# Kernel tuning notes

Measured on AMD Instinct MI355X. Metric: run time of the kernel, lower is better.

Reference implementation:

```python
import jax, jax.numpy as jnp
import numpy as np
import math

DIM = 1024
H = 16
DH = DIM // H
B = 2
L = 1024


def setup_inputs() -> dict:
    key = jax.random.key(0)
    ks = jax.random.split(key, 8)
    s = 1.0 / math.sqrt(DIM)
    return {
        "Q": jax.random.normal(ks[0], (B, L, DIM), jnp.float32),
        "K": jax.random.normal(ks[1], (B, L, DIM), jnp.float32),
        "mask_Q": jax.random.bernoulli(ks[2], 0.1, (B, L)),
        "mask_K": jax.random.bernoulli(ks[3], 0.1, (B, L)),
        "Wq": jax.random.normal(ks[4], (DIM, DIM), jnp.float32) * s,
        "Wk": jax.random.normal(ks[5], (DIM, DIM), jnp.float32) * s,
        "Wv": jax.random.normal(ks[6], (DIM, DIM), jnp.float32) * s,
        "Wo": jax.random.normal(ks[7], (DIM, DIM), jnp.float32) * s,
    }


def reference(Q, K, mask_Q, mask_K, Wq, Wk, Wv, Wo):
    # V defaults to K. Masked positions of inputs are zeroed first.
    Qz = jnp.where(mask_Q[:, :, None], 0.0, Q)
    Kz = jnp.where(mask_K[:, :, None], 0.0, K)
    Vz = Kz  # V = K, masked with mask_K

    # Projections (nn.Linear, no bias): y = x @ W.T
    Qp = jnp.einsum('bld,ed->ble', Qz, Wq)
    Kp = jnp.einsum('bld,ed->ble', Kz, Wk)
    Vp = jnp.einsum('bld,ed->ble', Vz, Wv)

    # split heads: [B, L, H, DH] -> per-head attention
    qh = Qp.reshape(B, L, H, DH)
    kh = Kp.reshape(B, L, H, DH)
    vh = Vp.reshape(B, L, H, DH)

    # NOTE: original scales by sqrt(dim) (full dim), not sqrt(dim_split)
    scores = jnp.einsum('bqhd,bkhd->bhqk', qh, kh) / math.sqrt(DIM)

    # outer-product validity mask: valid iff both q and k positions unmasked
    valid = (~mask_Q)[:, None, :, None] & (~mask_K)[:, None, None, :]  # [B,1,Lq,Lk]
    A = jnp.where(valid, scores, -1e38)
    A = jax.nn.softmax(A, axis=-1)
    A = jnp.where(valid, A, 0.0)

    O = jnp.einsum('bhqk,bkhd->bqhd', A, vh).reshape(B, L, DIM)
    # residual uses the PROJECTED Q (Q was reassigned to fc_q(Q) in torch)
    O = Qp + O
    # masked_forward(fc_o, ...): fc_o applied, masked query rows forced to 0
    ff = jax.nn.relu(jnp.where(mask_Q[:, :, None], 0.0, jnp.einsum('bld,ed->ble', O, Wo)))
    O = O + ff
    return O
```

## Files before the change

kernel.cpp:

```cpp
#include <hip/hip_runtime.h>
#include <hip/hip_bf16.h>


#define DEV __device__ __forceinline__

typedef __attribute__((ext_vector_type(8))) short bf16x8;
typedef __attribute__((ext_vector_type(4))) float f32x4;
typedef __hip_bfloat16 bf16;

DEV void glds16(const bf16* g, bf16* s) {
  __builtin_amdgcn_global_load_lds(
      (const __attribute__((address_space(1))) void*)g,
      (__attribute__((address_space(3))) void*)s, 16, 0, 0);
}

DEV unsigned short f2bu(float x) {
  __hip_bfloat16 b = __float2bfloat16(x);
  unsigned short u;
  __builtin_memcpy(&u, &b, 2);
  return u;
}

DEV float bu2f(unsigned short u) {
  unsigned int v = (unsigned int)u << 16;
  float f;
  __builtin_memcpy(&f, &v, 4);
  return f;
}

__global__ __launch_bounds__(256) void cast_all(
    const float* __restrict__ Q, const float* __restrict__ K,
    const unsigned char* __restrict__ mq_raw, const unsigned char* __restrict__ mk_raw,
    const float* __restrict__ W0, const float* __restrict__ W1,
    const float* __restrict__ W2, const float* __restrict__ W3,
    bf16* __restrict__ Qz, bf16* __restrict__ Kz,
    bf16* __restrict__ o0, bf16* __restrict__ o1,
    bf16* __restrict__ o2, bf16* __restrict__ o3,
    unsigned char* __restrict__ mqn,
    unsigned long long* __restrict__ qm64, unsigned long long* __restrict__ km64) {
  __shared__ int cnt;
  const int z = blockIdx.z;
  const int t = threadIdx.x;
  if (z < 2) {
    const float* X = z ? K : Q;
    const unsigned char* raw = z ? mk_raw : mq_raw;
    bf16* out = z ? Kz : Qz;
    if (t == 0) cnt = 0;
    __syncthreads();
    int c = 0;
#pragma unroll
    for (int j = 0; j < 8; ++j) c += (raw[t * 8 + j] != 0);
    atomicAdd(&cnt, c);
    __syncthreads();
    const bool isByte = cnt > 128;
    int i = (blockIdx.x * 256 + t) * 8;
    int row = i >> 10;
    bool masked = isByte ? (raw[row] != 0) : (((const int*)raw)[row] != 0);
    float4 v0 = *(const float4*)&X[i];
    float4 v1 = *(const float4*)&X[i + 4];
    if (masked) {
      v0 = make_float4(0.f, 0.f, 0.f, 0.f);
      v1 = make_float4(0.f, 0.f, 0.f, 0.f);
    }
    *(ushort4*)&out[i] = make_ushort4(f2bu(v0.x), f2bu(v0.y), f2bu(v0.z), f2bu(v0.w));
    *(ushort4*)&out[i + 4] = make_ushort4(f2bu(v1.x), f2bu(v1.y), f2bu(v1.z), f2bu(v1.w));
  } else if (z < 6) {
    if (blockIdx.x >= 512) return;
    const float* X; bf16* out;
    switch (z) {
      case 2: X = W0; out = o0; break;
      case 3: X = W1; out = o1; break;
      case 4: X = W2; out = o2; break;
      default: X = W3; out = o3; break;
    }
    int i = (blockIdx.x * 256 + t) * 8;
    float4 v0 = *(const float4*)&X[i];
    float4 v1 = *(const float4*)&X[i + 4];
    *(ushort4*)&out[i] = make_ushort4(f2bu(v0.x), f2bu(v0.y), f2bu(v0.z), f2bu(v0.w));
    *(ushort4*)&out[i + 4] = make_ushort4(f2bu(v1.x), f2bu(v1.y), f2bu(v1.z), f2bu(v1.w));
  } else {
    if (blockIdx.x != 0) return;
    if (t == 0) cnt = 0;
    __syncthreads();
    int c = 0;
    for (int i = t; i < 2048; i += 256) c += (mq_raw[i] != 0);
    atomicAdd(&cnt, c);
    __syncthreads();
    const bool isByte = cnt > 128;
    for (int i = t; i < 2048; i += 256)
      mqn[i] = isByte ? (mq_raw[i] != 0) : (((const int*)mq_raw)[i] != 0);
    if (t < 64) {
      const unsigned char* src = (t < 32) ? mk_raw : mq_raw;
      int idx = t & 31;
      unsigned long long m = 0;
      for (int j = 0; j < 64; ++j) {
        int pos = idx * 64 + j;
        bool bit = isByte ? (src[pos] != 0) : (((const int*)src)[pos] != 0);
        m |= (unsigned long long)bit << j;
      }
      if (t < 32) km64[idx] = m; else qm64[idx] = m;
    }
  }
}

template <int MI, int NI, typename EPI>
DEV void gemm_core(const bf16* __restrict__ A, const bf16* __restrict__ W,
                   int K, int brow, int bcol, EPI&& epi) {
  __shared__ bf16 As[2 * MI * 512];
  __shared__ bf16 Bs[2 * NI * 2048];
  const int t = threadIdx.x, l = t & 63, w = t >> 6;
  const int rs = l >> 2;
  const int kcol = (l & 3) * 8;

  f32x4 acc[MI][NI];
#pragma unroll
  for (int i = 0; i < MI; i++)
#pragma unroll
    for (int j = 0; j < NI; j++) acc[i][j] = (f32x4){0.f, 0.f, 0.f, 0.f};

  auto stage = [&](int k0, int b_) {
#pragma unroll
    for (int i = 0; i < MI; ++i)
      if ((i & 3) == w)
        glds16(A + (size_t)(brow + i * 16 + rs) * K + k0 + kcol,
               &As[b_ * MI * 512 + i * 512]);
#pragma unroll
    for (int c = 0; c < NI; ++c)
      glds16(W + (size_t)(bcol + (w * NI + c) * 16 + rs) * K + k0 + kcol,
             &Bs[b_ * NI * 2048 + (w * NI + c) * 512]);
  };

  const int aoff0 = (l & 15) * 32 + (l >> 4) * 8;
  const int boff0 = (w * NI * 16 + (l & 15)) * 32 + (l >> 4) * 8;

  stage(0, 0);
  int buf = 0;
  for (int k0 = 0; k0 < K; k0 += 32) {
    __syncthreads();
    if (k0 + 32 < K) stage(k0 + 32, buf ^ 1);
    bf16x8 a[MI], b[NI];
#pragma unroll
    for (int mi = 0; mi < MI; ++mi)
      a[mi] = *(const bf16x8*)&As[buf * MI * 512 + aoff0 + mi * 512];
#pragma unroll
    for (int ni = 0; ni < NI; ++ni)
      b[ni] = *(const bf16x8*)&Bs[buf * NI * 2048 + boff0 + ni * 512];
#pragma unroll
    for (int mi = 0; mi < MI; ++mi)
#pragma unroll
      for (int ni = 0; ni < NI; ++ni)
        acc[mi][ni] = __builtin_amdgcn_mfma_f32_16x16x32_bf16(a[mi], b[ni], acc[mi][ni], 0, 0, 0);
    buf ^= 1;
  }

#pragma unroll
  for (int mi = 0; mi < MI; ++mi)
#pragma unroll
    for (int ni = 0; ni < NI; ++ni)
#pragma unroll
      for (int r = 0; r < 4; ++r) {
        int row = brow + mi * 16 + (l >> 4) * 4 + r;
        int col = bcol + (w * NI + ni) * 16 + (l & 15);
        epi(row, col, acc[mi][ni][r]);
      }
}

__global__ __launch_bounds__(256) void proj_gemm(
    const bf16* __restrict__ Qz, const bf16* __restrict__ Kz,
    const bf16* __restrict__ Wq, const bf16* __restrict__ Wk, const bf16* __restrict__ Wv,
    bf16* __restrict__ Qpb, bf16* __restrict__ Kpb, bf16* __restrict__ Vpb) {
  const int z = blockIdx.z;
  const int brow = blockIdx.x * 32, bcol = blockIdx.y * 128;
  const bf16* A = (z == 0) ? Qz : Kz;
  const bf16* W = (z == 0) ? Wq : ((z == 1) ? Wk : Wv);
  bf16* dst = (z == 0) ? Qpb : ((z == 1) ? Kpb : Vpb);
  const float scale = (z == 0) ? 0.045084220f : 1.0f;
  gemm_core<2, 2>(A, W, 1024, brow, bcol, [&](int row, int col, float v) {
    dst[((size_t)row << 10) + col] = __float2bfloat16(v * scale);
  });
}

__global__ __launch_bounds__(256) void final_gemm(
    const bf16* __restrict__ Ob, const bf16* __restrict__ Wo,
    float* __restrict__ out, const unsigned char* __restrict__ mq) {
  const int brow = blockIdx.x * 32, bcol = blockIdx.y * 64;
  gemm_core<2, 1>(Ob, Wo, 1024, brow, bcol, [&](int row, int col, float v) {
    size_t idx = ((size_t)row << 10) + col;
    float ff = mq[row] ? 0.f : fmaxf(v, 0.f);
    out[idx] = out[idx] + ff;
  });
}

__global__ __launch_bounds__(512) void attn_fused(
    const bf16* __restrict__ Qpb, const bf16* __restrict__ Kpb, const bf16* __restrict__ Vpb,
    const unsigned long long* __restrict__ qm64, const unsigned long long* __restrict__ km64,
    float* __restrict__ Of, bf16* __restrict__ Ob) {
  __shared__ bf16 Klds[2][2][64 * 64];
  __shared__ bf16 Vt[2][64 * 72];
  __shared__ float CombO[256][17];
  __shared__ float CombP[256];

  const int t = threadIdx.x, l = t & 63, w = t >> 6;
  const int kg = w >> 2, wq = w & 3;
  const int tg = t & 255;
  const int q = l & 15, g = l >> 4;
  const int f = blockIdx.x;
  const int bh = (f & 7) + 8 * ((f >> 3) & 3);
  const int qt = f >> 5;
  const int b = bh >> 4, h = bh & 15;
  const size_t bbase = (size_t)b * 1024;

  const int qg = qt * 64 + wq * 16 + q;
  const bf16* qptr = Qpb + (bbase + qg) * 1024 + h * 64 + g * 8;
  const bf16x8 qb0 = *(const bf16x8*)qptr;
  const bf16x8 qb1 = *(const bf16x8*)(qptr + 32);

  float psum = 0.f;
  f32x4 oacc[4];
#pragma unroll
  for (int mf = 0; mf < 4; ++mf) oacc[mf] = (f32x4){0.f, 0.f, 0.f, 0.f};

  const int krow_s = l >> 3;
  const int kcol_s = ((l & 7) ^ krow_s) * 8;
  const int vk0 = 2 * (tg & 31);
  const int vdc = tg >> 5;

  union { uint4 v; unsigned short s[8]; } u0, u1;

  auto stageK = [&](int kt_, int b_) {
#pragma unroll
    for (int c = 0; c < 2; ++c) {
      int cw = wq * 2 + c;
      glds16(Kpb + (bbase + kt_ * 64 + cw * 8 + krow_s) * 1024 + h * 64 + kcol_s,
             &Klds[kg][b_][cw * 512]);
    }
  };
  auto loadV = [&](int kt_) {
    const bf16* g0 = Vpb + (bbase + kt_ * 64 + vk0) * 1024 + h * 64 + vdc * 8;
    u0.v = *(const uint4*)g0;
    u1.v = *(const uint4*)(g0 + 1024);
  };

  stageK(kg * 8, 0);
  loadV(kg * 8);
  int buf = 0;

  for (int it = 0; it < 8; ++it) {
    const int kt = kg * 8 + it;
    const unsigned long long km = km64[b * 16 + kt];
    const unsigned long long mloc = km >> (4 * g);

    __syncthreads();

#pragma unroll
    for (int j = 0; j < 8; ++j) {
      unsigned int pk = (unsigned int)u0.s[j] | ((unsigned int)u1.s[j] << 16);
      *(unsigned int*)((char*)&Vt[kg][0] + (vdc * 8 + j) * 144 + vk0 * 2) = pk;
    }

    f32x4 S[4];
#pragma unroll
    for (int mf = 0; mf < 4; ++mf) {
#pragma unroll
      for (int r = 0; r < 4; ++r)
        S[mf][r] = ((mloc >> (mf * 16 + r)) & 1ull) ? -1e30f : 0.f;
      const int row = mf * 16 + q;
      const int rowb = row * 128;
      const bf16x8 ka0 = *(const bf16x8*)((const char*)&Klds[kg][buf][0] + rowb + ((g ^ (row & 7)) * 16));
      const bf16x8 ka1 = *(const bf16x8*)((const char*)&Klds[kg][buf][0] + rowb + (((g + 4) ^ (row & 7)) * 16));
      S[mf] = __builtin_amdgcn_mfma_f32_16x16x32_bf16(ka0, qb0, S[mf], 0, 0, 0);
      S[mf] = __builtin_amdgcn_mfma_f32_16x16x32_bf16(ka1, qb1, S[mf], 0, 0, 0);
    }

    unsigned int lo[4], hi[4];
#pragma unroll
    for (int mf = 0; mf < 4; ++mf) {
      float p0 = exp2f(S[mf][0]), p1 = exp2f(S[mf][1]);
      float p2 = exp2f(S[mf][2]), p3 = exp2f(S[mf][3]);
      psum += (p0 + p1) + (p2 + p3);
      lo[mf] = (unsigned int)f2bu(p0) | ((unsigned int)f2bu(p1) << 16);
      hi[mf] = (unsigned int)f2bu(p2) | ((unsigned int)f2bu(p3) << 16);
    }

    __syncthreads();

    if (it < 7) {
      stageK(kt + 1, buf ^ 1);
      loadV(kt + 1);
    }

    const int srcA = ((2 * g) & 3) * 16 + q;
    const int srcB = srcA + 16;
    const bool sel = (g >> 1) & 1;
#pragma unroll
    for (int ks = 0; ks < 2; ++ks) {
      unsigned int a0 = __shfl(lo[2 * ks], srcA), a1 = __shfl(hi[2 * ks], srcA);
      unsigned int a2 = __shfl(lo[2 * ks], srcB), a3 = __shfl(hi[2 * ks], srcB);
      unsigned int b0 = __shfl(lo[2 * ks + 1], srcA), b1 = __shfl(hi[2 * ks + 1], srcA);
      unsigned int b2 = __shfl(lo[2 * ks + 1], srcB), b3 = __shfl(hi[2 * ks + 1], srcB);
      uint4 pw;
      pw.x = sel ? b0 : a0; pw.y = sel ? b1 : a1;
      pw.z = sel ? b2 : a2; pw.w = sel ? b3 : a3;
      const bf16x8 pa = __builtin_bit_cast(bf16x8, pw);
#pragma unroll
      for (int mf = 0; mf < 4; ++mf) {
        const bf16x8 va = *(const bf16x8*)((const char*)&Vt[kg][0] + (mf * 16 + q) * 144 + ks * 64 + g * 16);
        oacc[mf] = __builtin_amdgcn_mfma_f32_16x16x32_bf16(va, pa, oacc[mf], 0, 0, 0);
      }
    }
    buf ^= 1;
  }

  __syncthreads();
  if (t >= 256) {
#pragma unroll
    for (int mf = 0; mf < 4; ++mf)
#pragma unroll
      for (int r = 0; r < 4; ++r) CombO[tg][mf * 4 + r] = oacc[mf][r];
    CombP[tg] = psum;
  }
  __syncthreads();
  if (t < 256) {
#pragma unroll
    for (int mf = 0; mf < 4; ++mf)
#pragma unroll
      for (int r = 0; r < 4; ++r) oacc[mf][r] += CombO[t][mf * 4 + r];
    psum += CombP[t];
    psum += __shfl_xor(psum, 16);
    psum += __shfl_xor(psum, 32);

    const unsigned long long qm = qm64[b * 16 + qt];
    const bool qvalid = !((qm >> (wq * 16 + q)) & 1ull);
    const float inv = (qvalid && psum > 0.f) ? 1.f / psum : 0.f;
    const float RQ = 22.180709777918f;
#pragma unroll
    for (int mf = 0; mf < 4; ++mf) {
      size_t idx = (bbase + qg) * 1024 + h * 64 + mf * 16 + g * 4;
      ushort4 q4 = *(const ushort4*)&Qpb[idx];
      float4 val;
      val.x = bu2f(q4.x) * RQ + oacc[mf][0] * inv;
      val.y = bu2f(q4.y) * RQ + oacc[mf][1] * inv;
      val.z = bu2f(q4.z) * RQ + oacc[mf][2] * inv;
      val.w = bu2f(q4.w) * RQ + oacc[mf][3] * inv;
      *(float4*)&Of[idx] = val;
      *(ushort4*)&Ob[idx] = make_ushort4(f2bu(val.x), f2bu(val.y), f2bu(val.z), f2bu(val.w));
    }
  }
}

extern "C" void kernel_launch(void* const* d_in, const int* in_sizes, int n_in,
                              void* d_out, int out_size, void* d_ws, size_t ws_size,
                              hipStream_t stream) {
  const float* Q = (const float*)d_in[0];
  const float* K = (const float*)d_in[1];
  const unsigned char* mQraw = (const unsigned char*)d_in[2];
  const unsigned char* mKraw = (const unsigned char*)d_in[3];
  const float* Wq = (const float*)d_in[4];
  const float* Wk = (const float*)d_in[5];
  const float* Wv = (const float*)d_in[6];
  const float* Wo = (const float*)d_in[7];
  float* out = (float*)d_out;

  char* ws = (char*)d_ws;
  const size_t MB = 1024 * 1024;
  bf16* Qz = (bf16*)(ws + 0);
  bf16* Kz = (bf16*)(ws + 4 * MB);
  bf16* Wqb = (bf16*)(ws + 8 * MB);
  bf16* Wkb = (bf16*)(ws + 10 * MB);
  bf16* Wvb = (bf16*)(ws + 12 * MB);
  bf16* Wob = (bf16*)(ws + 14 * MB);
  bf16* Qpb = (bf16*)(ws + 16 * MB);
  bf16* Kpb = (bf16*)(ws + 20 * MB);
  bf16* Vpb = (bf16*)(ws + 24 * MB);
  bf16* Ob  = (bf16*)(ws + 28 * MB);
  unsigned char* mqn = (unsigned char*)(ws + 32 * MB);
  unsigned long long* km64 = (unsigned long long*)(ws + 32 * MB + 4096);
  unsigned long long* qm64 = km64 + 32;

  dim3 gc(1024, 1, 7);
  cast_all<<<gc, 256, 0, stream>>>(Q, K, mQraw, mKraw, Wq, Wk, Wv, Wo,
                                   Qz, Kz, Wqb, Wkb, Wvb, Wob, mqn, qm64, km64);

  dim3 gp(64, 8, 3);
  proj_gemm<<<gp, 256, 0, stream>>>(Qz, Kz, Wqb, Wkb, Wvb, Qpb, Kpb, Vpb);

  attn_fused<<<512, 512, 0, stream>>>(Qpb, Kpb, Vpb, qm64, km64, out, Ob);

  dim3 gf(64, 16);
  final_gemm<<<gf, 256, 0, stream>>>(Ob, Wob, out, mqn);
}
```

Before: 104.5 us.

## Retile projection and output GEMMs, add XCD-aware block mapping, drop attention key split

The projection GEMM moves to 128x128 tiles with 4x4 MFMA per wave, and the output GEMM to 64x64 tiles. Both use a 1D grid remapped so neighbouring tiles land on the same XCD. The attention kernel drops the two-way key split and its LDS combine step, running 256 threads over all 16 key tiles, and s_setprio is placed around the MFMA blocks. The aim is more operand reuse per tile, better L2 locality and no reduction overhead. The cost is fewer blocks in flight and longer serial loops in attention.

```diff
diff --git a/kernel.cpp b/kernel.cpp
--- a/kernel.cpp
+++ b/kernel.cpp
@@ -103,106 +103,141 @@
   }
 }
 
-template <int MI, int NI, typename EPI>
-DEV void gemm_core(const bf16* __restrict__ A, const bf16* __restrict__ W,
-                   int K, int brow, int bcol, EPI&& epi) {
-  __shared__ bf16 As[2 * MI * 512];
-  __shared__ bf16 Bs[2 * NI * 2048];
-  const int t = threadIdx.x, l = t & 63, w = t >> 6;
-  const int rs = l >> 2;
-  const int kcol = (l & 3) * 8;
-
-  f32x4 acc[MI][NI];
-#pragma unroll
-  for (int i = 0; i < MI; i++)
-#pragma unroll
-    for (int j = 0; j < NI; j++) acc[i][j] = (f32x4){0.f, 0.f, 0.f, 0.f};
-
-  auto stage = [&](int k0, int b_) {
-#pragma unroll
-    for (int i = 0; i < MI; ++i)
-      if ((i & 3) == w)
-        glds16(A + (size_t)(brow + i * 16 + rs) * K + k0 + kcol,
-               &As[b_ * MI * 512 + i * 512]);
-#pragma unroll
-    for (int c = 0; c < NI; ++c)
-      glds16(W + (size_t)(bcol + (w * NI + c) * 16 + rs) * K + k0 + kcol,
-             &Bs[b_ * NI * 2048 + (w * NI + c) * 512]);
-  };
-
-  const int aoff0 = (l & 15) * 32 + (l >> 4) * 8;
-  const int boff0 = (w * NI * 16 + (l & 15)) * 32 + (l >> 4) * 8;
-
-  stage(0, 0);
-  int buf = 0;
-  for (int k0 = 0; k0 < K; k0 += 32) {
-    __syncthreads();
-    if (k0 + 32 < K) stage(k0 + 32, buf ^ 1);
-    bf16x8 a[MI], b[NI];
-#pragma unroll
-    for (int mi = 0; mi < MI; ++mi)
-      a[mi] = *(const bf16x8*)&As[buf * MI * 512 + aoff0 + mi * 512];
-#pragma unroll
-    for (int ni = 0; ni < NI; ++ni)
-      b[ni] = *(const bf16x8*)&Bs[buf * NI * 2048 + boff0 + ni * 512];
-#pragma unroll
-    for (int mi = 0; mi < MI; ++mi)
-#pragma unroll
-      for (int ni = 0; ni < NI; ++ni)
-        acc[mi][ni] = __builtin_amdgcn_mfma_f32_16x16x32_bf16(a[mi], b[ni], acc[mi][ni], 0, 0, 0);
-    buf ^= 1;
-  }
-
-#pragma unroll
-  for (int mi = 0; mi < MI; ++mi)
-#pragma unroll
-    for (int ni = 0; ni < NI; ++ni)
-#pragma unroll
-      for (int r = 0; r < 4; ++r) {
-        int row = brow + mi * 16 + (l >> 4) * 4 + r;
-        int col = bcol + (w * NI + ni) * 16 + (l & 15);
-        epi(row, col, acc[mi][ni][r]);
-      }
-}
-
 __global__ __launch_bounds__(256) void proj_gemm(
     const bf16* __restrict__ Qz, const bf16* __restrict__ Kz,
     const bf16* __restrict__ Wq, const bf16* __restrict__ Wk, const bf16* __restrict__ Wv,
     bf16* __restrict__ Qpb, bf16* __restrict__ Kpb, bf16* __restrict__ Vpb) {
-  const int z = blockIdx.z;
-  const int brow = blockIdx.x * 32, bcol = blockIdx.y * 128;
+  __shared__ bf16 As[2][128 * 32];
+  __shared__ bf16 Bs[2][128 * 32];
+  const int raw = blockIdx.x;
+  const int xcd = raw & 7, idx = raw >> 3;
+  const int x = idx & 15;
+  const int g = (idx >> 4) * 8 + xcd;
+  const int y = g & 7, z = g >> 3;
   const bf16* A = (z == 0) ? Qz : Kz;
   const bf16* W = (z == 0) ? Wq : ((z == 1) ? Wk : Wv);
   bf16* dst = (z == 0) ? Qpb : ((z == 1) ? Kpb : Vpb);
   const float scale = (z == 0) ? 0.045084220f : 1.0f;
-  gemm_core<2, 2>(A, W, 1024, brow, bcol, [&](int row, int col, float v) {
-    dst[((size_t)row << 10) + col] = __float2bfloat16(v * scale);
-  });
+  const int brow = x * 128, bcol = y * 128;
+
+  const int t = threadIdx.x, l = t & 63, w = t >> 6;
+  const int wr = w >> 1, wc = w & 1;
+  const int rA0 = w * 32 + (l >> 2);
+  const int kcol = (l & 3) * 8;
+
+  f32x4 acc[4][4];
+#pragma unroll
+  for (int i = 0; i < 4; i++)
+#pragma unroll
+    for (int j = 0; j < 4; j++) acc[i][j] = (f32x4){0.f, 0.f, 0.f, 0.f};
+
+  auto stage = [&](int k0, int b_) {
+#pragma unroll
+    for (int c = 0; c < 2; ++c) {
+      glds16(A + (size_t)(brow + rA0 + c * 16) * 1024 + k0 + kcol,
+             &As[b_][w * 1024 + c * 512]);
+      glds16(W + (size_t)(bcol + rA0 + c * 16) * 1024 + k0 + kcol,
+             &Bs[b_][w * 1024 + c * 512]);
+    }
+  };
+
+  const int aoff = (wr * 64 + (l & 15)) * 32 + (l >> 4) * 8;
+  const int boff = (wc * 64 + (l & 15)) * 32 + (l >> 4) * 8;
+
+  stage(0, 0);
+  int buf = 0;
+  for (int k0 = 0; k0 < 1024; k0 += 32) {
+    __syncthreads();
+    if (k0 + 32 < 1024) stage(k0 + 32, buf ^ 1);
+    bf16x8 a[4], b[4];
+#pragma unroll
+    for (int mi = 0; mi < 4; ++mi) a[mi] = *(const bf16x8*)&As[buf][aoff + mi * 512];
+#pragma unroll
+    for (int ni = 0; ni < 4; ++ni) b[ni] = *(const bf16x8*)&Bs[buf][boff + ni * 512];
+    __builtin_amdgcn_s_setprio(1);
+#pragma unroll
+    for (int mi = 0; mi < 4; ++mi)
+#pragma unroll
+      for (int ni = 0; ni < 4; ++ni)
+        acc[mi][ni] = __builtin_amdgcn_mfma_f32_16x16x32_bf16(a[mi], b[ni], acc[mi][ni], 0, 0, 0);
+    __builtin_amdgcn_s_setprio(0);
+    buf ^= 1;
+  }
+
+#pragma unroll
+  for (int mi = 0; mi < 4; ++mi)
+#pragma unroll
+    for (int ni = 0; ni < 4; ++ni)
+#pragma unroll
+      for (int r = 0; r < 4; ++r) {
+        int row = brow + wr * 64 + mi * 16 + (l >> 4) * 4 + r;
+        int col = bcol + wc * 64 + ni * 16 + (l & 15);
+        dst[((size_t)row << 10) + col] = __float2bfloat16(acc[mi][ni][r] * scale);
+      }
 }
 
 __global__ __launch_bounds__(256) void final_gemm(
     const bf16* __restrict__ Ob, const bf16* __restrict__ Wo,
     float* __restrict__ out, const unsigned char* __restrict__ mq) {
-  const int brow = blockIdx.x * 32, bcol = blockIdx.y * 64;
-  gemm_core<2, 1>(Ob, Wo, 1024, brow, bcol, [&](int row, int col, float v) {
-    size_t idx = ((size_t)row << 10) + col;
-    float ff = mq[row] ? 0.f : fmaxf(v, 0.f);
-    out[idx] = out[idx] + ff;
-  });
-}
-
-__global__ __launch_bounds__(512) void attn_fused(
+  __shared__ bf16 As[2][64 * 32];
+  __shared__ bf16 Bs[2][64 * 32];
+  const int raw = blockIdx.x;
+  const int xcd = raw & 7, idx = raw >> 3;
+  const int x = idx & 31;
+  const int y = (idx >> 5) * 8 + xcd;
+  const int brow = x * 64, bcol = y * 64;
+
+  const int t = threadIdx.x, l = t & 63, w = t >> 6;
+  const int rs = l >> 2;
+  const int kcol = (l & 3) * 8;
+
+  f32x4 acc[4];
+#pragma unroll
+  for (int i = 0; i < 4; i++) acc[i] = (f32x4){0.f, 0.f, 0.f, 0.f};
+
+  auto stage = [&](int k0, int b_) {
+    glds16(Ob + (size_t)(brow + w * 16 + rs) * 1024 + k0 + kcol, &As[b_][w * 512]);
+    glds16(Wo + (size_t)(bcol + w * 16 + rs) * 1024 + k0 + kcol, &Bs[b_][w * 512]);
+  };
+
+  const int aoff = (l & 15) * 32 + (l >> 4) * 8;
+  const int boff = (w * 16 + (l & 15)) * 32 + (l >> 4) * 8;
+
+  stage(0, 0);
+  int buf = 0;
+  for (int k0 = 0; k0 < 1024; k0 += 32) {
+    __syncthreads();
+    if (k0 + 32 < 1024) stage(k0 + 32, buf ^ 1);
+    bf16x8 a[4], b;
+#pragma unroll
+    for (int mi = 0; mi < 4; ++mi) a[mi] = *(const bf16x8*)&As[buf][aoff + mi * 512];
+    b = *(const bf16x8*)&Bs[buf][boff];
+#pragma unroll
+    for (int mi = 0; mi < 4; ++mi)
+      acc[mi] = __builtin_amdgcn_mfma_f32_16x16x32_bf16(a[mi], b, acc[mi], 0, 0, 0);
+    buf ^= 1;
+  }
+
+#pragma unroll
+  for (int mi = 0; mi < 4; ++mi)
+#pragma unroll
+    for (int r = 0; r < 4; ++r) {
+      int row = brow + mi * 16 + (l >> 4) * 4 + r;
+      int col = bcol + w * 16 + (l & 15);
+      size_t idx2 = ((size_t)row << 10) + col;
+      float ff = mq[row] ? 0.f : fmaxf(acc[mi][r], 0.f);
+      out[idx2] = out[idx2] + ff;
+    }
+}
+
+__global__ __launch_bounds__(256) void attn_fused(
     const bf16* __restrict__ Qpb, const bf16* __restrict__ Kpb, const bf16* __restrict__ Vpb,
     const unsigned long long* __restrict__ qm64, const unsigned long long* __restrict__ km64,
     float* __restrict__ Of, bf16* __restrict__ Ob) {
-  __shared__ bf16 Klds[2][2][64 * 64];
-  __shared__ bf16 Vt[2][64 * 72];
-  __shared__ float CombO[256][17];
-  __shared__ float CombP[256];
+  __shared__ bf16 Klds[2][64 * 64];
+  __shared__ bf16 Vt[64 * 72];
 
   const int t = threadIdx.x, l = t & 63, w = t >> 6;
-  const int kg = w >> 2, wq = w & 3;
-  const int tg = t & 255;
   const int q = l & 15, g = l >> 4;
   const int f = blockIdx.x;
   const int bh = (f & 7) + 8 * ((f >> 3) & 3);
@@ -210,7 +245,7 @@
   const int b = bh >> 4, h = bh & 15;
   const size_t bbase = (size_t)b * 1024;
 
-  const int qg = qt * 64 + wq * 16 + q;
+  const int qg = qt * 64 + w * 16 + q;
   const bf16* qptr = Qpb + (bbase + qg) * 1024 + h * 64 + g * 8;
   const bf16x8 qb0 = *(const bf16x8*)qptr;
   const bf16x8 qb1 = *(const bf16x8*)(qptr + 32);
@@ -222,17 +257,17 @@
 
   const int krow_s = l >> 3;
   const int kcol_s = ((l & 7) ^ krow_s) * 8;
-  const int vk0 = 2 * (tg & 31);
-  const int vdc = tg >> 5;
+  const int vk0 = 2 * (t & 31);
+  const int vdc = t >> 5;
 
   union { uint4 v; unsigned short s[8]; } u0, u1;
 
   auto stageK = [&](int kt_, int b_) {
 #pragma unroll
     for (int c = 0; c < 2; ++c) {
-      int cw = wq * 2 + c;
+      int cw = w * 2 + c;
       glds16(Kpb + (bbase + kt_ * 64 + cw * 8 + krow_s) * 1024 + h * 64 + kcol_s,
-             &Klds[kg][b_][cw * 512]);
+             &Klds[b_][cw * 512]);
     }
   };
   auto loadV = [&](int kt_) {
@@ -241,12 +276,11 @@
     u1.v = *(const uint4*)(g0 + 1024);
   };
 
-  stageK(kg * 8, 0);
-  loadV(kg * 8);
+  stageK(0, 0);
+  loadV(0);
   int buf = 0;
 
-  for (int it = 0; it < 8; ++it) {
-    const int kt = kg * 8 + it;
+  for (int kt = 0; kt < 16; ++kt) {
     const unsigned long long km = km64[b * 16 + kt];
     const unsigned long long mloc = km >> (4 * g);
 
@@ -255,10 +289,11 @@
 #pragma unroll
     for (int j = 0; j < 8; ++j) {
       unsigned int pk = (unsigned int)u0.s[j] | ((unsigned int)u1.s[j] << 16);
-      *(unsigned int*)((char*)&Vt[kg][0] + (vdc * 8 + j) * 144 + vk0 * 2) = pk;
+      *(unsigned int*)((char*)Vt + (vdc * 8 + j) * 144 + vk0 * 2) = pk;
     }
 
     f32x4 S[4];
+    __builtin_amdgcn_s_setprio(1);
 #pragma unroll
     for (int mf = 0; mf < 4; ++mf) {
 #pragma unroll
@@ -266,11 +301,12 @@
         S[mf][r] = ((mloc >> (mf * 16 + r)) & 1ull) ? -1e30f : 0.f;
       const int row = mf * 16 + q;
       const int rowb = row * 128;
-      const bf16x8 ka0 = *(const bf16x8*)((const char*)&Klds[kg][buf][0] + rowb + ((g ^ (row & 7)) * 16));
-      const bf16x8 ka1 = *(const bf16x8*)((const char*)&Klds[kg][buf][0] + rowb + (((g + 4) ^ (row & 7)) * 16));
+      const bf16x8 ka0 = *(const bf16x8*)((const char*)&Klds[buf][0] + rowb + ((g ^ (row & 7)) * 16));
+      const bf16x8 ka1 = *(const bf16x8*)((const char*)&Klds[buf][0] + rowb + (((g + 4) ^ (row & 7)) * 16));
       S[mf] = __builtin_amdgcn_mfma_f32_16x16x32_bf16(ka0, qb0, S[mf], 0, 0, 0);
       S[mf] = __builtin_amdgcn_mfma_f32_16x16x32_bf16(ka1, qb1, S[mf], 0, 0, 0);
     }
+    __builtin_amdgcn_s_setprio(0);
 
     unsigned int lo[4], hi[4];
 #pragma unroll
@@ -284,7 +320,7 @@
 
     __syncthreads();
 
-    if (it < 7) {
+    if (kt < 15) {
       stageK(kt + 1, buf ^ 1);
       loadV(kt + 1);
     }
@@ -302,49 +338,35 @@
       pw.x = sel ? b0 : a0; pw.y = sel ? b1 : a1;
       pw.z = sel ? b2 : a2; pw.w = sel ? b3 : a3;
       const bf16x8 pa = __builtin_bit_cast(bf16x8, pw);
+      __builtin_amdgcn_s_setprio(1);
 #pragma unroll
       for (int mf = 0; mf < 4; ++mf) {
-        const bf16x8 va = *(const bf16x8*)((const char*)&Vt[kg][0] + (mf * 16 + q) * 144 + ks * 64 + g * 16);
+        const bf16x8 va = *(const bf16x8*)((const char*)Vt + (mf * 16 + q) * 144 + ks * 64 + g * 16);
         oacc[mf] = __builtin_amdgcn_mfma_f32_16x16x32_bf16(va, pa, oacc[mf], 0, 0, 0);
       }
+      __builtin_amdgcn_s_setprio(0);
     }
     buf ^= 1;
   }
 
-  __syncthreads();
-  if (t >= 256) {
-#pragma unroll
-    for (int mf = 0; mf < 4; ++mf)
-#pragma unroll
-      for (int r = 0; r < 4; ++r) CombO[tg][mf * 4 + r] = oacc[mf][r];
-    CombP[tg] = psum;
-  }
-  __syncthreads();
-  if (t < 256) {
-#pragma unroll
-    for (int mf = 0; mf < 4; ++mf)
-#pragma unroll
-      for (int r = 0; r < 4; ++r) oacc[mf][r] += CombO[t][mf * 4 + r];
-    psum += CombP[t];
-    psum += __shfl_xor(psum, 16);
-    psum += __shfl_xor(psum, 32);
-
-    const unsigned long long qm = qm64[b * 16 + qt];
-    const bool qvalid = !((qm >> (wq * 16 + q)) & 1ull);
-    const float inv = (qvalid && psum > 0.f) ? 1.f / psum : 0.f;
-    const float RQ = 22.180709777918f;
-#pragma unroll
-    for (int mf = 0; mf < 4; ++mf) {
-      size_t idx = (bbase + qg) * 1024 + h * 64 + mf * 16 + g * 4;
-      ushort4 q4 = *(const ushort4*)&Qpb[idx];
-      float4 val;
-      val.x = bu2f(q4.x) * RQ + oacc[mf][0] * inv;
-      val.y = bu2f(q4.y) * RQ + oacc[mf][1] * inv;
-      val.z = bu2f(q4.z) * RQ + oacc[mf][2] * inv;
-      val.w = bu2f(q4.w) * RQ + oacc[mf][3] * inv;
-      *(float4*)&Of[idx] = val;
-      *(ushort4*)&Ob[idx] = make_ushort4(f2bu(val.x), f2bu(val.y), f2bu(val.z), f2bu(val.w));
-    }
+  psum += __shfl_xor(psum, 16);
+  psum += __shfl_xor(psum, 32);
+
+  const unsigned long long qm = qm64[b * 16 + qt];
+  const bool qvalid = !((qm >> (w * 16 + q)) & 1ull);
+  const float inv = (qvalid && psum > 0.f) ? 1.f / psum : 0.f;
+  const float RQ = 22.180709777918f;
+#pragma unroll
+  for (int mf = 0; mf < 4; ++mf) {
+    size_t idx = (bbase + qg) * 1024 + h * 64 + mf * 16 + g * 4;
+    ushort4 q4 = *(const ushort4*)&Qpb[idx];
+    float4 val;
+    val.x = bu2f(q4.x) * RQ + oacc[mf][0] * inv;
+    val.y = bu2f(q4.y) * RQ + oacc[mf][1] * inv;
+    val.z = bu2f(q4.z) * RQ + oacc[mf][2] * inv;
+    val.w = bu2f(q4.w) * RQ + oacc[mf][3] * inv;
+    *(float4*)&Of[idx] = val;
+    *(ushort4*)&Ob[idx] = make_ushort4(f2bu(val.x), f2bu(val.y), f2bu(val.z), f2bu(val.w));
   }
 }
 
@@ -363,8 +385,8 @@
 
   char* ws = (char*)d_ws;
   const size_t MB = 1024 * 1024;
-  bf16* Qz = (bf16*)(ws + 0);
-  bf16* Kz = (bf16*)(ws + 4 * MB);
+  bf16* Qz  = (bf16*)(ws + 0);
+  bf16* Kz  = (bf16*)(ws + 4 * MB);
   bf16* Wqb = (bf16*)(ws + 8 * MB);
   bf16* Wkb = (bf16*)(ws + 10 * MB);
   bf16* Wvb = (bf16*)(ws + 12 * MB);
@@ -381,11 +403,9 @@
   cast_all<<<gc, 256, 0, stream>>>(Q, K, mQraw, mKraw, Wq, Wk, Wv, Wo,
                                    Qz, Kz, Wqb, Wkb, Wvb, Wob, mqn, qm64, km64);
 
-  dim3 gp(64, 8, 3);
-  proj_gemm<<<gp, 256, 0, stream>>>(Qz, Kz, Wqb, Wkb, Wvb, Qpb, Kpb, Vpb);
-
-  attn_fused<<<512, 512, 0, stream>>>(Qpb, Kpb, Vpb, qm64, km64, out, Ob);
-
-  dim3 gf(64, 16);
-  final_gemm<<<gf, 256, 0, stream>>>(Ob, Wob, out, mqn);
-}
+  proj_gemm<<<384, 256, 0, stream>>>(Qz, Kz, Wqb, Wkb, Wvb, Qpb, Kpb, Vpb);
+
+  attn_fused<<<512, 256, 0, stream>>>(Qpb, Kpb, Vpb, qm64, km64, out, Ob);
+
+  final_gemm<<<512, 256, 0, stream>>>(Ob, Wob, out, mqn);
+}
```

New measurement: 101.2 us. 3.1% less time.

## Enlarge GEMM row tiles and restructure attention to 256 threads with paired key tiles

Applied to the files above, without the earlier changes.

The projection and output GEMMs now use 64-row tiles (MI=4) instead of 32, halving grid size and increasing per-block reuse of weight tiles. The attention kernel drops the two key-group split across 8 waves and its LDS combine step; instead 4 waves each process two key tiles per iteration, covering all 16 key tiles serially. This removes the cross-group reduction and shared buffers but halves threads per block and doubles serial loop length per wave, reducing latency hiding in attention.

```diff
diff --git a/kernel.cpp b/kernel.cpp
--- a/kernel.cpp
+++ b/kernel.cpp
@@ -170,12 +170,12 @@
     const bf16* __restrict__ Wq, const bf16* __restrict__ Wk, const bf16* __restrict__ Wv,
     bf16* __restrict__ Qpb, bf16* __restrict__ Kpb, bf16* __restrict__ Vpb) {
   const int z = blockIdx.z;
-  const int brow = blockIdx.x * 32, bcol = blockIdx.y * 128;
+  const int brow = blockIdx.x * 64, bcol = blockIdx.y * 128;
   const bf16* A = (z == 0) ? Qz : Kz;
   const bf16* W = (z == 0) ? Wq : ((z == 1) ? Wk : Wv);
   bf16* dst = (z == 0) ? Qpb : ((z == 1) ? Kpb : Vpb);
   const float scale = (z == 0) ? 0.045084220f : 1.0f;
-  gemm_core<2, 2>(A, W, 1024, brow, bcol, [&](int row, int col, float v) {
+  gemm_core<4, 2>(A, W, 1024, brow, bcol, [&](int row, int col, float v) {
     dst[((size_t)row << 10) + col] = __float2bfloat16(v * scale);
   });
 }
@@ -183,26 +183,22 @@
 __global__ __launch_bounds__(256) void final_gemm(
     const bf16* __restrict__ Ob, const bf16* __restrict__ Wo,
     float* __restrict__ out, const unsigned char* __restrict__ mq) {
-  const int brow = blockIdx.x * 32, bcol = blockIdx.y * 64;
-  gemm_core<2, 1>(Ob, Wo, 1024, brow, bcol, [&](int row, int col, float v) {
+  const int brow = blockIdx.x * 64, bcol = blockIdx.y * 64;
+  gemm_core<4, 1>(Ob, Wo, 1024, brow, bcol, [&](int row, int col, float v) {
     size_t idx = ((size_t)row << 10) + col;
     float ff = mq[row] ? 0.f : fmaxf(v, 0.f);
     out[idx] = out[idx] + ff;
   });
 }
 
-__global__ __launch_bounds__(512) void attn_fused(
+__global__ __launch_bounds__(256) void attn_fused(
     const bf16* __restrict__ Qpb, const bf16* __restrict__ Kpb, const bf16* __restrict__ Vpb,
     const unsigned long long* __restrict__ qm64, const unsigned long long* __restrict__ km64,
     float* __restrict__ Of, bf16* __restrict__ Ob) {
   __shared__ bf16 Klds[2][2][64 * 64];
   __shared__ bf16 Vt[2][64 * 72];
-  __shared__ float CombO[256][17];
-  __shared__ float CombP[256];
 
   const int t = threadIdx.x, l = t & 63, w = t >> 6;
-  const int kg = w >> 2, wq = w & 3;
-  const int tg = t & 255;
   const int q = l & 15, g = l >> 4;
   const int f = blockIdx.x;
   const int bh = (f & 7) + 8 * ((f >> 3) & 3);
@@ -210,7 +206,7 @@
   const int b = bh >> 4, h = bh & 15;
   const size_t bbase = (size_t)b * 1024;
 
-  const int qg = qt * 64 + wq * 16 + q;
+  const int qg = qt * 64 + w * 16 + q;
   const bf16* qptr = Qpb + (bbase + qg) * 1024 + h * 64 + g * 8;
   const bf16x8 qb0 = *(const bf16x8*)qptr;
   const bf16x8 qb1 = *(const bf16x8*)(qptr + 32);
@@ -222,42 +218,34 @@
 
   const int krow_s = l >> 3;
   const int kcol_s = ((l & 7) ^ krow_s) * 8;
-  const int vk0 = 2 * (tg & 31);
-  const int vdc = tg >> 5;
-
-  union { uint4 v; unsigned short s[8]; } u0, u1;
-
-  auto stageK = [&](int kt_, int b_) {
+  const int vk0 = 2 * (t & 31);
+  const int vdc = t >> 5;
+
+  union U { uint4 v; unsigned short s[8]; };
+  U uA0, uA1, uB0, uB1;
+
+  auto stageK = [&](int kt_, int b_, int half) {
 #pragma unroll
     for (int c = 0; c < 2; ++c) {
-      int cw = wq * 2 + c;
+      int cw = w * 2 + c;
       glds16(Kpb + (bbase + kt_ * 64 + cw * 8 + krow_s) * 1024 + h * 64 + kcol_s,
-             &Klds[kg][b_][cw * 512]);
-    }
-  };
-  auto loadV = [&](int kt_) {
+             &Klds[b_][half][cw * 512]);
+    }
+  };
+  auto loadV = [&](int kt_, U& x0, U& x1) {
     const bf16* g0 = Vpb + (bbase + kt_ * 64 + vk0) * 1024 + h * 64 + vdc * 8;
-    u0.v = *(const uint4*)g0;
-    u1.v = *(const uint4*)(g0 + 1024);
-  };
-
-  stageK(kg * 8, 0);
-  loadV(kg * 8);
-  int buf = 0;
-
-  for (int it = 0; it < 8; ++it) {
-    const int kt = kg * 8 + it;
-    const unsigned long long km = km64[b * 16 + kt];
-    const unsigned long long mloc = km >> (4 * g);
-
-    __syncthreads();
-
+    x0.v = *(const uint4*)g0;
+    x1.v = *(const uint4*)(g0 + 1024);
+  };
+  auto writeVt = [&](int half, U& x0, U& x1) {
 #pragma unroll
     for (int j = 0; j < 8; ++j) {
-      unsigned int pk = (unsigned int)u0.s[j] | ((unsigned int)u1.s[j] << 16);
-      *(unsigned int*)((char*)&Vt[kg][0] + (vdc * 8 + j) * 144 + vk0 * 2) = pk;
-    }
-
+      unsigned int pk = (unsigned int)x0.s[j] | ((unsigned int)x1.s[j] << 16);
+      *(unsigned int*)((char*)&Vt[half][0] + (vdc * 8 + j) * 144 + vk0 * 2) = pk;
+    }
+  };
+  auto qk_half = [&](const bf16* Kl, unsigned long long mloc,
+                     unsigned int* lo, unsigned int* hi) {
     f32x4 S[4];
 #pragma unroll
     for (int mf = 0; mf < 4; ++mf) {
@@ -266,13 +254,11 @@
         S[mf][r] = ((mloc >> (mf * 16 + r)) & 1ull) ? -1e30f : 0.f;
       const int row = mf * 16 + q;
       const int rowb = row * 128;
-      const bf16x8 ka0 = *(const bf16x8*)((const char*)&Klds[kg][buf][0] + rowb + ((g ^ (row & 7)) * 16));
-      const bf16x8 ka1 = *(const bf16x8*)((const char*)&Klds[kg][buf][0] + rowb + (((g + 4) ^ (row & 7)) * 16));
+      const bf16x8 ka0 = *(const bf16x8*)((const char*)Kl + rowb + ((g ^ (row & 7)) * 16));
+      const bf16x8 ka1 = *(const bf16x8*)((const char*)Kl + rowb + (((g + 4) ^ (row & 7)) * 16));
       S[mf] = __builtin_amdgcn_mfma_f32_16x16x32_bf16(ka0, qb0, S[mf], 0, 0, 0);
       S[mf] = __builtin_amdgcn_mfma_f32_16x16x32_bf16(ka1, qb1, S[mf], 0, 0, 0);
     }
-
-    unsigned int lo[4], hi[4];
 #pragma unroll
     for (int mf = 0; mf < 4; ++mf) {
       float p0 = exp2f(S[mf][0]), p1 = exp2f(S[mf][1]);
@@ -281,17 +267,11 @@
       lo[mf] = (unsigned int)f2bu(p0) | ((unsigned int)f2bu(p1) << 16);
       hi[mf] = (unsigned int)f2bu(p2) | ((unsigned int)f2bu(p3) << 16);
     }
-
-    __syncthreads();
-
-    if (it < 7) {
-      stageK(kt + 1, buf ^ 1);
-      loadV(kt + 1);
-    }
-
-    const int srcA = ((2 * g) & 3) * 16 + q;
-    const int srcB = srcA + 16;
-    const bool sel = (g >> 1) & 1;
+  };
+  const int srcA = ((2 * g) & 3) * 16 + q;
+  const int srcB = srcA + 16;
+  const bool sel = (g >> 1) & 1;
+  auto pv_half = [&](const bf16* Vl, unsigned int* lo, unsigned int* hi) {
 #pragma unroll
     for (int ks = 0; ks < 2; ++ks) {
       unsigned int a0 = __shfl(lo[2 * ks], srcA), a1 = __shfl(hi[2 * ks], srcA);
@@ -304,47 +284,63 @@
       const bf16x8 pa = __builtin_bit_cast(bf16x8, pw);
 #pragma unroll
       for (int mf = 0; mf < 4; ++mf) {
-        const bf16x8 va = *(const bf16x8*)((const char*)&Vt[kg][0] + (mf * 16 + q) * 144 + ks * 64 + g * 16);
+        const bf16x8 va = *(const bf16x8*)((const char*)Vl + (mf * 16 + q) * 144 + ks * 64 + g * 16);
         oacc[mf] = __builtin_amdgcn_mfma_f32_16x16x32_bf16(va, pa, oacc[mf], 0, 0, 0);
       }
     }
+  };
+
+  stageK(0, 0, 0);
+  stageK(1, 0, 1);
+  loadV(0, uA0, uA1);
+  loadV(1, uB0, uB1);
+  int buf = 0;
+
+  for (int p = 0; p < 8; ++p) {
+    const unsigned long long mloc0 = km64[b * 16 + 2 * p] >> (4 * g);
+    const unsigned long long mloc1 = km64[b * 16 + 2 * p + 1] >> (4 * g);
+
+    __syncthreads();
+
+    writeVt(0, uA0, uA1);
+    writeVt(1, uB0, uB1);
+
+    unsigned int lo0[4], hi0[4], lo1[4], hi1[4];
+    qk_half(&Klds[buf][0][0], mloc0, lo0, hi0);
+    qk_half(&Klds[buf][1][0], mloc1, lo1, hi1);
+
+    __syncthreads();
+
+    if (p < 7) {
+      stageK(2 * p + 2, buf ^ 1, 0);
+      stageK(2 * p + 3, buf ^ 1, 1);
+      loadV(2 * p + 2, uA0, uA1);
+      loadV(2 * p + 3, uB0, uB1);
+    }
+
+    pv_half(&Vt[0][0], lo0, hi0);
+    pv_half(&Vt[1][0], lo1, hi1);
     buf ^= 1;
   }
 
-  __syncthreads();
-  if (t >= 256) {
-#pragma unroll
-    for (int mf = 0; mf < 4; ++mf)
-#pragma unroll
-      for (int r = 0; r < 4; ++r) CombO[tg][mf * 4 + r] = oacc[mf][r];
-    CombP[tg] = psum;
-  }
-  __syncthreads();
-  if (t < 256) {
-#pragma unroll
-    for (int mf = 0; mf < 4; ++mf)
-#pragma unroll
-      for (int r = 0; r < 4; ++r) oacc[mf][r] += CombO[t][mf * 4 + r];
-    psum += CombP[t];
-    psum += __shfl_xor(psum, 16);
-    psum += __shfl_xor(psum, 32);
-
-    const unsigned long long qm = qm64[b * 16 + qt];
-    const bool qvalid = !((qm >> (wq * 16 + q)) & 1ull);
-    const float inv = (qvalid && psum > 0.f) ? 1.f / psum : 0.f;
-    const float RQ = 22.180709777918f;
-#pragma unroll
-    for (int mf = 0; mf < 4; ++mf) {
-      size_t idx = (bbase + qg) * 1024 + h * 64 + mf * 16 + g * 4;
-      ushort4 q4 = *(const ushort4*)&Qpb[idx];
-      float4 val;
-      val.x = bu2f(q4.x) * RQ + oacc[mf][0] * inv;
-      val.y = bu2f(q4.y) * RQ + oacc[mf][1] * inv;
-      val.z = bu2f(q4.z) * RQ + oacc[mf][2] * inv;
-      val.w = bu2f(q4.w) * RQ + oacc[mf][3] * inv;
-      *(float4*)&Of[idx] = val;
-      *(ushort4*)&Ob[idx] = make_ushort4(f2bu(val.x), f2bu(val.y), f2bu(val.z), f2bu(val.w));
-    }
+  psum += __shfl_xor(psum, 16);
+  psum += __shfl_xor(psum, 32);
+
+  const unsigned long long qm = qm64[b * 16 + qt];
+  const bool qvalid = !((qm >> (w * 16 + q)) & 1ull);
+  const float inv = (qvalid && psum > 0.f) ? 1.f / psum : 0.f;
+  const float RQ = 22.180709777918f;
+#pragma unroll
+  for (int mf = 0; mf < 4; ++mf) {
+    size_t idx = (bbase + qg) * 1024 + h * 64 + mf * 16 + g * 4;
+    ushort4 q4 = *(const ushort4*)&Qpb[idx];
+    float4 val;
+    val.x = bu2f(q4.x) * RQ + oacc[mf][0] * inv;
+    val.y = bu2f(q4.y) * RQ + oacc[mf][1] * inv;
+    val.z = bu2f(q4.z) * RQ + oacc[mf][2] * inv;
+    val.w = bu2f(q4.w) * RQ + oacc[mf][3] * inv;
+    *(float4*)&Of[idx] = val;
+    *(ushort4*)&Ob[idx] = make_ushort4(f2bu(val.x), f2bu(val.y), f2bu(val.z), f2bu(val.w));
   }
 }
 
@@ -363,8 +359,8 @@
 
   char* ws = (char*)d_ws;
   const size_t MB = 1024 * 1024;
-  bf16* Qz = (bf16*)(ws + 0);
-  bf16* Kz = (bf16*)(ws + 4 * MB);
+  bf16* Qz  = (bf16*)(ws + 0);
+  bf16* Kz  = (bf16*)(ws + 4 * MB);
   bf16* Wqb = (bf16*)(ws + 8 * MB);
   bf16* Wkb = (bf16*)(ws + 10 * MB);
   bf16* Wvb = (bf16*)(ws + 12 * MB);
@@ -381,11 +377,11 @@
   cast_all<<<gc, 256, 0, stream>>>(Q, K, mQraw, mKraw, Wq, Wk, Wv, Wo,
                                    Qz, Kz, Wqb, Wkb, Wvb, Wob, mqn, qm64, km64);
 
-  dim3 gp(64, 8, 3);
+  dim3 gp(32, 8, 3);
   proj_gemm<<<gp, 256, 0, stream>>>(Qz, Kz, Wqb, Wkb, Wvb, Qpb, Kpb, Vpb);
 
-  attn_fused<<<512, 512, 0, stream>>>(Qpb, Kpb, Vpb, qm64, km64, out, Ob);
-
-  dim3 gf(64, 16);
+  attn_fused<<<512, 256, 0, stream>>>(Qpb, Kpb, Vpb, qm64, km64, out, Ob);
+
+  dim3 gf(32, 16);
   final_gemm<<<gf, 256, 0, stream>>>(Ob, Wob, out, mqn);
 }
```

After: 100.6 us. 1.04x faster.
